# Kernel optimization log

Measured on AMD Instinct MI355X. Metric: run time of the kernel, lower is better.

## Reference

```python
import jax, jax.numpy as jnp
import numpy as np

B, S, D, H = 4, 1024, 1024, 16
HD = D // H
LN_EPS = 1e-5


def setup_inputs() -> dict:
    key = jax.random.key(0)
    k_x, k_win, k_wout = jax.random.split(key, 3)
    x = jax.random.normal(k_x, (B, S, D), dtype=jnp.float32)
    # nn.MultiheadAttention packed in-projection: (3*D, D)
    w_in = jax.random.normal(k_win, (3 * D, D), dtype=jnp.float32) * (1.0 / np.sqrt(D))
    b_in = jnp.zeros((3 * D,), dtype=jnp.float32)
    w_out = jax.random.normal(k_wout, (D, D), dtype=jnp.float32) * (1.0 / np.sqrt(D))
    b_out = jnp.zeros((D,), dtype=jnp.float32)
    ln_w = jnp.ones((D,), dtype=jnp.float32)
    ln_b = jnp.zeros((D,), dtype=jnp.float32)
    # causal mask: True = position is NOT allowed to attend (torch bool attn_mask semantics)
    attn_mask = jnp.triu(jnp.ones((S, S), dtype=bool), k=1)
    return {"x": x, "w_in": w_in, "b_in": b_in, "w_out": w_out,
            "b_out": b_out, "ln_w": ln_w, "ln_b": ln_b, "attn_mask": attn_mask}


def reference(x, w_in, b_in, w_out, b_out, ln_w, ln_b, attn_mask):
    # Pre-LN (biased variance, as torch LayerNorm)
    mu = jnp.mean(x, axis=-1, keepdims=True)
    var = jnp.mean(jnp.square(x - mu), axis=-1, keepdims=True)
    xn = (x - mu) * jax.lax.rsqrt(var + LN_EPS) * ln_w + ln_b

    # packed QKV projection
    qkv = xn @ w_in.T + b_in                      # (B, S, 3D)
    q, k, v = jnp.split(qkv, 3, axis=-1)
    # (B, S, D) -> (B, H, S, HD)
    to_heads = lambda t: t.reshape(B, S, H, HD).transpose(0, 2, 1, 3)
    q, k, v = to_heads(q), to_heads(k), to_heads(v)

    scores = jnp.einsum("bhqd,bhkd->bhqk", q, k) * (1.0 / np.sqrt(HD))
    scores = jnp.where(attn_mask, -jnp.inf, scores)
    weights = jax.nn.softmax(scores, axis=-1)     # (B, H, S, S) — need_weights, not averaged

    attn = jnp.einsum("bhqk,bhkd->bhqd", weights, v)
    attn = attn.transpose(0, 2, 1, 3).reshape(B, S, D)
    out = attn @ w_out.T + b_out

    return x + out, weights
```

## Files before the change

kernel.cpp:

```cpp
#include <hip/hip_runtime.h>


typedef __attribute__((ext_vector_type(8))) __bf16 bf16x8;
typedef __attribute__((ext_vector_type(4))) float f32x4;
typedef __attribute__((ext_vector_type(4))) unsigned short us4;

typedef const __attribute__((address_space(1))) void* gas_cvp;
typedef __attribute__((address_space(3))) void* las_vp;

static __device__ __forceinline__ unsigned short f2bf(float f) {
  union { float f; unsigned int u; } v; v.f = f;
  return (unsigned short)((v.u + 0x7fffu + ((v.u >> 16) & 1u)) >> 16);
}

static __device__ __forceinline__ f32x4 mfma16(bf16x8 a, bf16x8 b, f32x4 c) {
  return __builtin_amdgcn_mfma_f32_16x16x32_bf16(a, b, c, 0, 0, 0);
}

static __device__ __forceinline__ void gl_lds16(const void* g, void* l) {
  __builtin_amdgcn_global_load_lds((gas_cvp)g, (las_vp)l, 16, 0, 0);
}

static __device__ __forceinline__ int swz(int row) {
  return (((row & 3) ^ ((row >> 2) & 3)) << 4);
}

__global__ __launch_bounds__(256) void ln_cvt_kernel(const float* __restrict__ x,
    const float* __restrict__ lw, const float* __restrict__ lb,
    unsigned short* __restrict__ xn,
    const float* __restrict__ w_in, const float* __restrict__ w_out,
    unsigned short* __restrict__ dst) {
  if (blockIdx.x < 1024) {
    const int wave = threadIdx.x >> 6, lane = threadIdx.x & 63;
    const int row = blockIdx.x * 4 + wave;
    const float* xr = x + (size_t)row * 1024;
    f32x4 vals[4];
    float s = 0.f, s2 = 0.f;
#pragma unroll
    for (int c = 0; c < 4; ++c) {
      vals[c] = *(const f32x4*)(xr + (lane + 64 * c) * 4);
#pragma unroll
      for (int j = 0; j < 4; ++j) { s += vals[c][j]; s2 += vals[c][j] * vals[c][j]; }
    }
#pragma unroll
    for (int off = 32; off; off >>= 1) { s += __shfl_xor(s, off); s2 += __shfl_xor(s2, off); }
    const float mu = s * (1.f / 1024.f);
    const float var = s2 * (1.f / 1024.f) - mu * mu;
    const float rs = rsqrtf(var + 1e-5f);
    unsigned short* xo = xn + (size_t)row * 1024;
#pragma unroll
    for (int c = 0; c < 4; ++c) {
      const int e0 = (lane + 64 * c) * 4;
      f32x4 w = *(const f32x4*)(lw + e0);
      f32x4 b = *(const f32x4*)(lb + e0);
      us4 o;
#pragma unroll
      for (int j = 0; j < 4; ++j) o[j] = f2bf((vals[c][j] - mu) * rs * w[j] + b[j]);
      *(us4*)(xo + e0) = o;
    }
  } else {
    const int NW4 = (3072 * 1024) / 4;
    const int NT4 = NW4 + (1024 * 1024) / 4;
    for (int i = (blockIdx.x - 1024) * 256 + threadIdx.x; i < NT4; i += 1024 * 256) {
      f32x4 v = (i < NW4) ? ((const f32x4*)w_in)[i] : ((const f32x4*)w_out)[i - NW4];
      us4 o;
#pragma unroll
      for (int j = 0; j < 4; ++j) o[j] = f2bf(v[j]);
      ((us4*)dst)[i] = o;
    }
  }
}

__global__ __launch_bounds__(256) void qkv_gemm(const unsigned short* __restrict__ xn,
    const unsigned short* __restrict__ wb, const float* __restrict__ b_in,
    unsigned short* __restrict__ qw, unsigned short* __restrict__ kw,
    unsigned short* __restrict__ vt, float* __restrict__ wts) {
  __shared__ __align__(16) char As[2][8192];
  __shared__ __align__(16) char Bs[2][8192];
  const int tid = threadIdx.x;
  const int wave = tid >> 6, lane = tid & 63;
  const int g = lane >> 4, cL = lane & 15;
  const int m0 = blockIdx.x * 128, n0 = blockIdx.y * 128;
  const int wm = (wave >> 1) * 64, wn = (wave & 1) * 64;
  const int flat = blockIdx.y * 32 + blockIdx.x;

  f32x4 acc[4][4];
#pragma unroll
  for (int i = 0; i < 4; ++i)
#pragma unroll
    for (int j = 0; j < 4; ++j) acc[i][j] = (f32x4){0.f, 0.f, 0.f, 0.f};

  const char* xb = (const char*)xn;
  const char* wbb = (const char*)wb;

  auto stage = [&](int buf, int st) {
    const int k0b = st * 64;
#pragma unroll
    for (int i = 0; i < 2; ++i) {
      const int base = i * 4096 + wave * 1024;
      const int L = base + lane * 16;
      const int row = L >> 6, bb2 = L & 63;
      const int kb = bb2 ^ swz(row);
      gl_lds16(xb + (size_t)(m0 + row) * 2048 + k0b + kb, As[buf] + base);
      gl_lds16(wbb + (size_t)(n0 + row) * 2048 + k0b + kb, Bs[buf] + base);
    }
  };

  auto compute = [&](int buf) {
    bf16x8 af[4], bfm[4];
    const int kb = (g * 16) ^ (((cL & 3) ^ ((cL >> 2) & 3)) << 4);
#pragma unroll
    for (int mi = 0; mi < 4; ++mi) {
      af[mi] = *(const bf16x8*)(As[buf] + (wm + mi * 16 + cL) * 64 + kb);
      bfm[mi] = *(const bf16x8*)(Bs[buf] + (wn + mi * 16 + cL) * 64 + kb);
    }
#pragma unroll
    for (int mi = 0; mi < 4; ++mi)
#pragma unroll
      for (int ni = 0; ni < 4; ++ni)
        acc[mi][ni] = mfma16(bfm[ni], af[mi], acc[mi][ni]);
  };

  auto zero_tile = [&](int t) {
    const int head = t / 120;
    int r = t - head * 120;
    int zq = 0;
    while (r >= 15 - zq) { r -= 15 - zq; ++zq; }
    const int ct = zq + 1 + r;
    float* base = wts + ((size_t)head << 20) + ((size_t)(zq * 64) << 10) + ct * 64;
    const f32x4 z = {0.f, 0.f, 0.f, 0.f};
#pragma unroll
    for (int i = 0; i < 4; ++i) {
      const int row = wave * 16 + i * 4 + (lane >> 4);
      __builtin_nontemporal_store(z, (f32x4*)(base + ((size_t)row << 10) + (lane & 15) * 4));
    }
  };

  stage(0, 0);
  int cur = 0;
  int zi = 0;
  for (int st = 0; st < 31; ++st) {
    __syncthreads();
    stage(cur ^ 1, st + 1);
    if (st % 3 == 1 && zi < 10) zero_tile(flat * 10 + zi++);
    compute(cur);
    cur ^= 1;
  }
  __syncthreads();
  compute(cur);

  const int sect = n0 >> 10;
#pragma unroll
  for (int ni = 0; ni < 4; ++ni) {
    const int n_abs0 = n0 + wn + ni * 16 + g * 4;
    const f32x4 bias = *(const f32x4*)(b_in + n_abs0);
    const int nl0 = n_abs0 & 1023;
    const int h = nl0 >> 6, hd0 = nl0 & 63;
#pragma unroll
    for (int mi = 0; mi < 4; ++mi) {
      const int m_abs = m0 + wm + mi * 16 + cL;
      const int b = m_abs >> 10, sI = m_abs & 1023;
      const size_t bhI = (size_t)(b * 16 + h);
      us4 o;
#pragma unroll
      for (int r = 0; r < 4; ++r) o[r] = f2bf(acc[mi][ni][r] + bias[r]);
      if (sect == 0) {
        *(us4*)(qw + (bhI << 16) + ((size_t)sI << 6) + hd0) = o;
      } else if (sect == 1) {
        *(us4*)(kw + (bhI << 16) + ((size_t)sI << 6) + hd0) = o;
      } else {
#pragma unroll
        for (int r = 0; r < 4; ++r)
          vt[(bhI << 16) + ((size_t)(hd0 + r) << 10) + sI] = o[r];
      }
    }
  }
}

__global__ __launch_bounds__(256) void attn_kernel(const unsigned short* __restrict__ qw,
    const unsigned short* __restrict__ kw, const unsigned short* __restrict__ vt,
    unsigned short* __restrict__ attn, float* __restrict__ wts) {
  __shared__ __align__(16) char Ks[2][8192];
  __shared__ __align__(16) char Vs[2][8192];
  __shared__ __align__(16) unsigned short plds[4][16][40];
  const int tid = threadIdx.x, wave = tid >> 6, lane = tid & 63;
  const int g = lane >> 4, cL = lane & 15;
  const int bh = blockIdx.x & 63;
  const int u = blockIdx.x >> 6;
  const int qt = (u < 4) ? (15 - u) : (u < 8) ? (4 + u) : (u < 12) ? (15 - u) : (u - 12);
  const unsigned short* qh = qw + ((size_t)bh << 16);
  const char* khB = (const char*)(kw + ((size_t)bh << 16));
  const char* vhB = (const char*)(vt + ((size_t)bh << 16));
  unsigned short* ao = attn + ((size_t)bh << 16);
  float* wb = wts + ((size_t)bh << 20);
  const float sc2 = 0.125f * 1.44269504088896f;

  const int q0 = qt * 64 + wave * 16;
  const int ktd = q0 >> 4;
  const int nch = qt + 1;

  auto stageK = [&](int ch, int buf) {
#pragma unroll
    for (int i = 0; i < 2; ++i) {
      const int L = wave * 1024 + i * 4096 + lane * 16;
      const int r = L >> 7, c = (L >> 4) & 7;
      gl_lds16(khB + (size_t)(ch * 64 + r) * 128 + ((c ^ (r & 7)) << 4),
               Ks[buf] + wave * 1024 + i * 4096);
    }
  };
  auto stageV = [&](int ch, int buf) {
#pragma unroll
    for (int i = 0; i < 2; ++i) {
      const int L = wave * 1024 + i * 4096 + lane * 16;
      const int r = L >> 7, c = (L >> 4) & 7;
      gl_lds16(vhB + (size_t)r * 2048 + ch * 128 + ((c ^ (r & 7)) << 4),
               Vs[buf] + wave * 1024 + i * 4096);
    }
  };

  stageK(0, 0);

  const unsigned short* qp = qh + ((size_t)(q0 + cL) << 6) + g * 8;
  const bf16x8 bq0 = *(const bf16x8*)qp;
  const bf16x8 bq1 = *(const bf16x8*)(qp + 32);

  const int sw = cL & 7;
  const int kO0 = ((g ^ sw) << 4);
  const int kO1 = (((4 + g) ^ sw) << 4);

  float l = 0.f;
  for (int ch = 0; ch < nch; ++ch) {
    __syncthreads();
    if (ch + 1 < nch) stageK(ch + 1, (ch + 1) & 1);
    const char* kbuf = Ks[ch & 1];
#pragma unroll
    for (int tl = 0; tl < 4; ++tl) {
      const int kt = (ch << 2) + tl;
      if (kt > ktd) break;
      const char* kr = kbuf + ((tl << 4) + cL) * 128;
      const bf16x8 a0 = *(const bf16x8*)(kr + kO0);
      const bf16x8 a1 = *(const bf16x8*)(kr + kO1);
      f32x4 cf = mfma16(a1, bq1, mfma16(a0, bq0, (f32x4){0.f, 0.f, 0.f, 0.f}));
      if (kt < ktd) {
        l += exp2f(cf[0] * sc2) + exp2f(cf[1] * sc2) +
             exp2f(cf[2] * sc2) + exp2f(cf[3] * sc2);
      } else {
#pragma unroll
        for (int r = 0; r < 4; ++r)
          l += exp2f((g * 4 + r <= cL) ? cf[r] * sc2 : -1e30f);
      }
    }
  }
  l += __shfl_xor(l, 16);
  l += __shfl_xor(l, 32);
  const float inv = 1.f / l;

  f32x4 av[4];
#pragma unroll
  for (int i = 0; i < 4; ++i) av[i] = (f32x4){0.f, 0.f, 0.f, 0.f};
  __syncthreads();
  stageK(0, 0);
  stageV(0, 0);
  for (int ch = 0; ch < nch; ++ch) {
    __syncthreads();
    if (ch + 1 < nch) { stageK(ch + 1, (ch + 1) & 1); stageV(ch + 1, (ch + 1) & 1); }
    const int buf = ch & 1;
    const char* kbuf = Ks[buf];
#pragma unroll
    for (int tl = 0; tl < 4; ++tl) {
      const int kt = (ch << 2) + tl;
      f32x4 p4;
      if (kt <= ktd) {
        const char* kr = kbuf + ((tl << 4) + cL) * 128;
        const bf16x8 a0 = *(const bf16x8*)(kr + kO0);
        const bf16x8 a1 = *(const bf16x8*)(kr + kO1);
        f32x4 cf = mfma16(a1, bq1, mfma16(a0, bq0, (f32x4){0.f, 0.f, 0.f, 0.f}));
        const bool isd = (kt == ktd);
#pragma unroll
        for (int r = 0; r < 4; ++r) {
          const float v = (isd && (g * 4 + r > cL)) ? -1e30f : cf[r] * sc2;
          p4[r] = exp2f(v) * inv;
        }
      } else {
        p4 = (f32x4){0.f, 0.f, 0.f, 0.f};
      }
      *(f32x4*)(wb + ((size_t)(q0 + cL) << 10) + kt * 16 + g * 4) = p4;
      us4 pb;
#pragma unroll
      for (int r = 0; r < 4; ++r) pb[r] = f2bf(p4[r]);
      *(us4*)(&plds[wave][cL][(tl & 1) * 16 + g * 4]) = pb;
      if (tl & 1) {
        const int p = tl >> 1;
        const bf16x8 ap = *(const bf16x8*)(&plds[wave][cL][g * 8]);
#pragma unroll
        for (int ni = 0; ni < 4; ++ni) {
          const int rV = ni * 16 + cL;
          const bf16x8 bv = *(const bf16x8*)(Vs[buf] + rV * 128 +
                                             ((((p << 2) + g) ^ sw) << 4));
          av[ni] = mfma16(ap, bv, av[ni]);
        }
      }
    }
  }

#pragma unroll
  for (int ni = 0; ni < 4; ++ni)
#pragma unroll
    for (int r = 0; r < 4; ++r)
      ao[((size_t)(q0 + g * 4 + r) << 6) + ni * 16 + cL] = f2bf(av[ni][r]);
}

__global__ __launch_bounds__(256) void oproj_gemm(const unsigned short* __restrict__ attn,
    const unsigned short* __restrict__ wob, const float* __restrict__ b_out,
    const float* __restrict__ x, float* __restrict__ out0) {
  __shared__ __align__(16) char As[2][4096];
  __shared__ __align__(16) char Bs[2][8192];
  const int tid = threadIdx.x;
  const int wave = tid >> 6, lane = tid & 63;
  const int g = lane >> 4, cL = lane & 15;
  const int m0 = blockIdx.x * 64, n0 = blockIdx.y * 128;
  const int wm = (wave >> 1) * 32, wn = (wave & 1) * 64;

  f32x4 acc[2][4];
#pragma unroll
  for (int i = 0; i < 2; ++i)
#pragma unroll
    for (int j = 0; j < 4; ++j) acc[i][j] = (f32x4){0.f, 0.f, 0.f, 0.f};

  const char* ab = (const char*)attn;
  const char* wbb = (const char*)wob;

  auto stage = [&](int buf, int st) {
    const int h0 = st >> 1;
    const int inhead = (st & 1) * 64;
    {
      const int L = wave * 1024 + lane * 16;
      const int row = L >> 6, bb2 = L & 63;
      const int kb = bb2 ^ swz(row);
      const int m_abs = m0 + row;
      const int b = m_abs >> 10, sI = m_abs & 1023;
      gl_lds16(ab + ((((size_t)(b * 16 + h0)) << 10) + sI) * 128 + inhead + kb,
               As[buf] + wave * 1024);
    }
#pragma unroll
    for (int i = 0; i < 2; ++i) {
      const int base = i * 4096 + wave * 1024;
      const int L = base + lane * 16;
      const int row = L >> 6, bb2 = L & 63;
      const int kb = bb2 ^ swz(row);
      gl_lds16(wbb + (size_t)(n0 + row) * 2048 + st * 64 + kb, Bs[buf] + base);
    }
  };

  auto compute = [&](int buf) {
    bf16x8 af[2], bfm[4];
    const int kb = (g * 16) ^ (((cL & 3) ^ ((cL >> 2) & 3)) << 4);
#pragma unroll
    for (int mi = 0; mi < 2; ++mi)
      af[mi] = *(const bf16x8*)(As[buf] + (wm + mi * 16 + cL) * 64 + kb);
#pragma unroll
    for (int ni = 0; ni < 4; ++ni)
      bfm[ni] = *(const bf16x8*)(Bs[buf] + (wn + ni * 16 + cL) * 64 + kb);
#pragma unroll
    for (int mi = 0; mi < 2; ++mi)
#pragma unroll
      for (int ni = 0; ni < 4; ++ni)
        acc[mi][ni] = mfma16(bfm[ni], af[mi], acc[mi][ni]);
  };

  stage(0, 0);
  int cur = 0;
  for (int st = 0; st < 31; ++st) {
    __syncthreads();
    stage(cur ^ 1, st + 1);
    compute(cur);
    cur ^= 1;
  }
  __syncthreads();
  compute(cur);

#pragma unroll
  for (int ni = 0; ni < 4; ++ni) {
    const int n_abs0 = n0 + wn + ni * 16 + g * 4;
    const f32x4 bias = *(const f32x4*)(b_out + n_abs0);
#pragma unroll
    for (int mi = 0; mi < 2; ++mi) {
      const int m_abs = m0 + wm + mi * 16 + cL;
      const size_t idx = (size_t)m_abs * 1024 + n_abs0;
      const f32x4 xr = *(const f32x4*)(x + idx);
      f32x4 o;
#pragma unroll
      for (int r = 0; r < 4; ++r) o[r] = acc[mi][ni][r] + bias[r] + xr[r];
      *(f32x4*)(out0 + idx) = o;
    }
  }
}

extern "C" void kernel_launch(void* const* d_in, const int* in_sizes, int n_in,
                              void* d_out, int out_size, void* d_ws, size_t ws_size,
                              hipStream_t stream) {
  const float* x     = (const float*)d_in[0];
  const float* w_in  = (const float*)d_in[1];
  const float* b_in  = (const float*)d_in[2];
  const float* w_out = (const float*)d_in[3];
  const float* b_out = (const float*)d_in[4];
  const float* ln_w  = (const float*)d_in[5];
  const float* ln_b  = (const float*)d_in[6];

  char* ws = (char*)d_ws;
  unsigned short* xn  = (unsigned short*)(ws);
  unsigned short* wcb = (unsigned short*)(ws + ((size_t)8  << 20));
  unsigned short* qw  = (unsigned short*)(ws + ((size_t)16 << 20));
  unsigned short* kw  = (unsigned short*)(ws + ((size_t)24 << 20));
  unsigned short* vt  = (unsigned short*)(ws + ((size_t)32 << 20));
  unsigned short* at  = (unsigned short*)(ws + ((size_t)40 << 20));
  unsigned short* wib = wcb;
  unsigned short* wob = wcb + (size_t)3072 * 1024;

  float* out0 = (float*)d_out;
  float* wts  = out0 + (size_t)4096 * 1024;

  ln_cvt_kernel<<<2048, 256, 0, stream>>>(x, ln_w, ln_b, xn, w_in, w_out, wcb);
  qkv_gemm<<<dim3(32, 24), 256, 0, stream>>>(xn, wib, b_in, qw, kw, vt, wts);
  attn_kernel<<<1024, 256, 0, stream>>>(qw, kw, vt, at, wts);
  oproj_gemm<<<dim3(64, 8), 256, 0, stream>>>(at, wob, b_out, x, out0);
}
```

Measured before the change: 132.9 us.

## Fuse two-pass softmax into one pass with deferred normalization via weight rescale

Drops the separate pass that only computed row sums of exp(scores). The main loop now writes unnormalized probabilities to the weights output, accumulates the row sum alongside, and then rescales the written weights row by reading them back, while the P·V accumulator is scaled by 1/l at the end. This saves one full QK^T plus exp pass and one round of K staging, at the cost of an extra read-modify-write of the fp32 weights matrix in global memory. No running max is subtracted, which the code before also omitted, so numerical behaviour is unchanged.

```diff
diff --git a/kernel.cpp b/kernel.cpp
--- a/kernel.cpp
+++ b/kernel.cpp
@@ -219,6 +219,7 @@
   };
 
   stageK(0, 0);
+  stageV(0, 0);
 
   const unsigned short* qp = qh + ((size_t)(q0 + cL) << 6) + g * 8;
   const bf16x8 bq0 = *(const bf16x8*)qp;
@@ -229,38 +230,10 @@
   const int kO1 = (((4 + g) ^ sw) << 4);
 
   float l = 0.f;
-  for (int ch = 0; ch < nch; ++ch) {
-    __syncthreads();
-    if (ch + 1 < nch) stageK(ch + 1, (ch + 1) & 1);
-    const char* kbuf = Ks[ch & 1];
-#pragma unroll
-    for (int tl = 0; tl < 4; ++tl) {
-      const int kt = (ch << 2) + tl;
-      if (kt > ktd) break;
-      const char* kr = kbuf + ((tl << 4) + cL) * 128;
-      const bf16x8 a0 = *(const bf16x8*)(kr + kO0);
-      const bf16x8 a1 = *(const bf16x8*)(kr + kO1);
-      f32x4 cf = mfma16(a1, bq1, mfma16(a0, bq0, (f32x4){0.f, 0.f, 0.f, 0.f}));
-      if (kt < ktd) {
-        l += exp2f(cf[0] * sc2) + exp2f(cf[1] * sc2) +
-             exp2f(cf[2] * sc2) + exp2f(cf[3] * sc2);
-      } else {
-#pragma unroll
-        for (int r = 0; r < 4; ++r)
-          l += exp2f((g * 4 + r <= cL) ? cf[r] * sc2 : -1e30f);
-      }
-    }
-  }
-  l += __shfl_xor(l, 16);
-  l += __shfl_xor(l, 32);
-  const float inv = 1.f / l;
-
   f32x4 av[4];
 #pragma unroll
   for (int i = 0; i < 4; ++i) av[i] = (f32x4){0.f, 0.f, 0.f, 0.f};
-  __syncthreads();
-  stageK(0, 0);
-  stageV(0, 0);
+
   for (int ch = 0; ch < nch; ++ch) {
     __syncthreads();
     if (ch + 1 < nch) { stageK(ch + 1, (ch + 1) & 1); stageV(ch + 1, (ch + 1) & 1); }
@@ -269,7 +242,7 @@
 #pragma unroll
     for (int tl = 0; tl < 4; ++tl) {
       const int kt = (ch << 2) + tl;
-      f32x4 p4;
+      f32x4 pt;
       if (kt <= ktd) {
         const char* kr = kbuf + ((tl << 4) + cL) * 128;
         const bf16x8 a0 = *(const bf16x8*)(kr + kO0);
@@ -279,15 +252,16 @@
 #pragma unroll
         for (int r = 0; r < 4; ++r) {
           const float v = (isd && (g * 4 + r > cL)) ? -1e30f : cf[r] * sc2;
-          p4[r] = exp2f(v) * inv;
+          pt[r] = exp2f(v);
+          l += pt[r];
         }
       } else {
-        p4 = (f32x4){0.f, 0.f, 0.f, 0.f};
+        pt = (f32x4){0.f, 0.f, 0.f, 0.f};
       }
-      *(f32x4*)(wb + ((size_t)(q0 + cL) << 10) + kt * 16 + g * 4) = p4;
+      *(f32x4*)(wb + ((size_t)(q0 + cL) << 10) + kt * 16 + g * 4) = pt;
       us4 pb;
 #pragma unroll
-      for (int r = 0; r < 4; ++r) pb[r] = f2bf(p4[r]);
+      for (int r = 0; r < 4; ++r) pb[r] = f2bf(pt[r]);
       *(us4*)(&plds[wave][cL][(tl & 1) * 16 + g * 4]) = pb;
       if (tl & 1) {
         const int p = tl >> 1;
@@ -303,11 +277,28 @@
     }
   }
 
+  l += __shfl_xor(l, 16);
+  l += __shfl_xor(l, 32);
+  const float inv = 1.f / l;
+
+  {
+    float* prow = wb + ((size_t)(q0 + cL) << 10) + g * 4;
+    for (int kt = 0; kt <= ktd; ++kt) {
+      f32x4 v = *(const f32x4*)(prow + kt * 16);
+#pragma unroll
+      for (int r = 0; r < 4; ++r) v[r] *= inv;
+      *(f32x4*)(prow + kt * 16) = v;
+    }
+  }
+
+  float invr[4];
+#pragma unroll
+  for (int r = 0; r < 4; ++r) invr[r] = __shfl(inv, g * 4 + r);
 #pragma unroll
   for (int ni = 0; ni < 4; ++ni)
 #pragma unroll
     for (int r = 0; r < 4; ++r)
-      ao[((size_t)(q0 + g * 4 + r) << 6) + ni * 16 + cL] = f2bf(av[ni][r]);
+      ao[((size_t)(q0 + g * 4 + r) << 6) + ni * 16 + cL] = f2bf(av[ni][r] * invr[r]);
 }
 
 __global__ __launch_bounds__(256) void oproj_gemm(const unsigned short* __restrict__ attn,
```

Result: slower. 164.2 us (+23.6%).
